# Performance work log

Hardware: AMD Instinct MI355X
Metric: run time of the kernel (lower is better)

The kernel has to match this reference:

```python
import jax, jax.numpy as jnp
import numpy as np

B, SEQ, D_TOK = 2, 2048, 1536
H, DH = 24, 64
TP, NS, NMH, DFLOW = 4, 256, 8, 64


def setup_inputs() -> dict:
    key = jax.random.key(0)
    ks = jax.random.split(key, 10)
    s = 0.02  # weight scale to keep activations sane
    return {
        "hidden_states": jax.random.normal(ks[0], (B, SEQ, D_TOK), jnp.float32),
        "Wq": jax.random.normal(ks[1], (D_TOK, D_TOK), jnp.float32) * s,
        "Wk": jax.random.normal(ks[2], (D_TOK, D_TOK), jnp.float32) * s,
        "Wv": jax.random.normal(ks[3], (D_TOK, D_TOK), jnp.float32) * s,
        "Wo": jax.random.normal(ks[4], (D_TOK, D_TOK), jnp.float32) * s,
        "bo": jnp.zeros((D_TOK,), jnp.float32),
        "M": jax.random.normal(ks[5], (B, TP, NS, DFLOW), jnp.float32),
        "W_region": jax.random.uniform(ks[6], (B, TP, NS, 1), jnp.float32),
        "Fk": jax.random.normal(ks[7], (NMH, DFLOW, DH), jnp.float32) * s,
        "Fv": jax.random.normal(ks[8], (NMH, DFLOW, DH), jnp.float32) * s,
    }


def reference(hidden_states, Wq, Wk, Wv, Wo, bo, M, W_region, Fk, Fv):
    # QKV projections, split into heads: [B, H, seq, Dh]
    Q = (hidden_states @ Wq).reshape(B, SEQ, H, DH).transpose(0, 2, 1, 3)
    K = (hidden_states @ Wk).reshape(B, SEQ, H, DH).transpose(0, 2, 1, 3)
    V = (hidden_states @ Wv).reshape(B, SEQ, H, DH).transpose(0, 2, 1, 3)

    # Motion injection (vectorized over b, h, t): region-gated flow deltas
    # delta[b,h,t,n,d] = W_region[b,t,n] * (M[b,t,n,:] @ Fk[h])
    gate = W_region[:, None]  # [B,1,TP,NS,1]
    dK = jnp.einsum('btnf,hfd->bhtnd', M, Fk) * gate  # [B,NMH,TP,NS,DH]
    dV = jnp.einsum('btnf,hfd->bhtnd', M, Fv) * gate

    # seq = 2 blocks (content, canny) x TP frames x NS spatial tokens;
    # delta is applied to both halves of each frame, first NMH heads only.
    K = K.reshape(B, H, 2, TP, NS, DH).at[:, :NMH].add(dK[:, :, None]).reshape(B, H, SEQ, DH)
    V = V.reshape(B, H, 2, TP, NS, DH).at[:, :NMH].add(dV[:, :, None]).reshape(B, H, SEQ, DH)

    # Standard SDPA
    scale = 1.0 / np.sqrt(DH).astype(np.float32)
    scores = jnp.einsum('bhqd,bhkd->bhqk', Q, K) * scale
    attn_w = jax.nn.softmax(scores, axis=-1)
    out = jnp.einsum('bhqk,bhkd->bhqd', attn_w, V)

    out = out.transpose(0, 2, 1, 3).reshape(B, SEQ, D_TOK)
    return out @ Wo + bo
```

## Files before the change

### kernel.cpp

```cpp
#include <hip/hip_runtime.h>
#include <hip/hip_bf16.h>

typedef __attribute__((ext_vector_type(4))) float f32x4;
typedef __attribute__((ext_vector_type(8))) short bf16x8;

#define LOG2E 1.4426950408889634f

__device__ __forceinline__ unsigned short f2b(float f) {
  union { float f; unsigned u; } v; v.f = f;
  unsigned r = v.u + 0x7fffu + ((v.u >> 16) & 1u);
  return (unsigned short)(r >> 16);
}
__device__ __forceinline__ float b2f(unsigned short s) {
  union { unsigned u; float f; } v; v.u = ((unsigned)s) << 16;
  return v.f;
}
__device__ __forceinline__ unsigned cvtpk(float lo, float hi) {
  unsigned r;
  asm("v_cvt_pk_bf16_f32 %0, %1, %2" : "=v"(r) : "v"(lo), "v"(hi));
  return r;
}
__device__ __forceinline__ float fexp2(float x) {
  float r;
  asm("v_exp_f32 %0, %1" : "=v"(r) : "v"(x));
  return r;
}

__device__ __forceinline__ void gload_lds16(const void* g, void* l) {
  __builtin_amdgcn_global_load_lds(
      (const __attribute__((address_space(1))) unsigned*)g,
      (__attribute__((address_space(3))) unsigned*)l, 16, 0, 0);
}

__global__ __launch_bounds__(256) void k_cvt(const float* __restrict__ src,
                                             unsigned short* __restrict__ dst, int n4) {
  int i = blockIdx.x * 256 + threadIdx.x;
  if (i >= n4) return;
  float4 v = ((const float4*)src)[i];
  ushort4 o;
  o.x = f2b(v.x); o.y = f2b(v.y); o.z = f2b(v.z); o.w = f2b(v.w);
  ((ushort4*)dst)[i] = o;
}

__global__ __launch_bounds__(256) void k_transpose(const float* __restrict__ src,
                                                   unsigned short* __restrict__ dst) {
  __shared__ float tile[64][65];
  const int tx = threadIdx.x & 63, ty = threadIdx.x >> 6;
  const int r0 = (blockIdx.x / 24) * 64, c0 = (blockIdx.x % 24) * 64;
#pragma unroll
  for (int j = 0; j < 16; ++j)
    tile[ty + j * 4][tx] = src[(size_t)(r0 + ty + j * 4) * 1536 + c0 + tx];
  __syncthreads();
#pragma unroll
  for (int j = 0; j < 16; ++j)
    dst[(size_t)(c0 + ty + j * 4) * 1536 + r0 + tx] = f2b(tile[tx][ty + j * 4]);
}

template <int OUTBF16>
__global__ __launch_bounds__(256) void k_gemm(const unsigned short* __restrict__ A,
                                              const unsigned short* __restrict__ BT,
                                              void* __restrict__ C,
                                              const float* __restrict__ bias,
                                              int M, int N, int K, int gridN) {
  __shared__ unsigned short As[128 * 32];
  __shared__ unsigned short Bs[128 * 32];
  const int tid = threadIdx.x;
  const int lane = tid & 63, wave = tid >> 6;
  const int bm = (blockIdx.x / gridN) * 128;
  const int bn = (blockIdx.x % gridN) * 128;
  const int wr = (wave >> 1) * 64, wc = (wave & 1) * 64;
  const int r15 = lane & 15, g = lane >> 4;
  const int row0 = tid >> 2, c0 = tid & 3;

  f32x4 acc[4][4] = {};

  for (int k0 = 0; k0 < K; k0 += 32) {
    __syncthreads();
    gload_lds16(A + (size_t)(bm + row0) * K + k0 + c0 * 8, (char*)As + wave * 1024);
    gload_lds16(A + (size_t)(bm + row0 + 64) * K + k0 + c0 * 8,
                (char*)As + 4096 + wave * 1024);
    gload_lds16(BT + (size_t)(bn + row0) * K + k0 + c0 * 8, (char*)Bs + wave * 1024);
    gload_lds16(BT + (size_t)(bn + row0 + 64) * K + k0 + c0 * 8,
                (char*)Bs + 4096 + wave * 1024);
    __syncthreads();
    bf16x8 af[4], bfr[4];
#pragma unroll
    for (int m = 0; m < 4; ++m) {
      af[m] = *(const bf16x8*)&As[(wr + m * 16 + r15) * 32 + g * 8];
      bfr[m] = *(const bf16x8*)&Bs[(wc + m * 16 + r15) * 32 + g * 8];
    }
#pragma unroll
    for (int m = 0; m < 4; ++m)
#pragma unroll
      for (int n = 0; n < 4; ++n)
        acc[m][n] = __builtin_amdgcn_mfma_f32_16x16x32_bf16(af[m], bfr[n], acc[m][n], 0, 0, 0);
  }

#pragma unroll
  for (int m = 0; m < 4; ++m)
#pragma unroll
    for (int n = 0; n < 4; ++n)
#pragma unroll
      for (int i = 0; i < 4; ++i) {
        int row = bm + wr + m * 16 + g * 4 + i;
        int col = bn + wc + n * 16 + r15;
        float v = acc[m][n][i];
        if (OUTBF16)
          ((unsigned short*)C)[(size_t)row * N + col] = f2b(v);
        else
          ((float*)C)[(size_t)row * N + col] = v + bias[col];
      }
}

__global__ __launch_bounds__(256) void k_inject(const float* __restrict__ Mm,
                                                const float* __restrict__ Wr,
                                                const float* __restrict__ Fk,
                                                const float* __restrict__ Fv,
                                                unsigned short* __restrict__ qkv) {
  __shared__ float Ml[256];
  __shared__ float gl[4];
  const int bid = blockIdx.x;
  const int nb = bid & 63, t = (bid >> 6) & 3, h = (bid >> 8) & 7, b = bid >> 11;
  const int tid = threadIdx.x;
  const int nl = tid >> 6, d = tid & 63;
  Ml[tid] = Mm[(size_t)(((b * 4 + t) * 256 + nb * 4) * 64) + tid];
  if (tid < 4) gl[tid] = Wr[(b * 4 + t) * 256 + nb * 4 + tid];
  __syncthreads();
  float ak = 0.f, av = 0.f;
#pragma unroll 8
  for (int f = 0; f < 64; ++f) {
    float mv = Ml[nl * 64 + f];
    ak += mv * Fk[(h * 64 + f) * 64 + d];
    av += mv * Fv[(h * 64 + f) * 64 + d];
  }
  float gate = gl[nl];
  ak *= gate; av *= gate;
  const int n = nb * 4 + nl;
  const size_t s0 = (size_t)(b * 2048 + t * 256 + n);
#pragma unroll
  for (int r = 0; r < 2; ++r) {
    size_t row = s0 + (size_t)r * 1024;
    size_t ik = row * 4608 + 1536 + h * 64 + d;
    qkv[ik] = f2b(b2f(qkv[ik]) + ak);
    size_t iv = row * 4608 + 3072 + h * 64 + d;
    qkv[iv] = f2b(b2f(qkv[iv]) + av);
  }
}

__global__ __launch_bounds__(512) void k_attn(const unsigned short* __restrict__ qkv,
                                              unsigned short* __restrict__ attno) {
  __shared__ unsigned short Kl[64 * 64];
  __shared__ unsigned short VT[64 * 72];
  __shared__ unsigned short Pl[8][16 * 72];
  const int tid = threadIdx.x;
  const int lane = tid & 63, wave = tid >> 6;
  const int bid = blockIdx.x;
  const int qt = bid & 15;
  const int h = (bid >> 4) % 24;
  const int b = (bid >> 4) / 24;
  const int r15 = lane & 15, g = lane >> 4, sw7 = lane & 7;
  const int q0 = qt * 128 + wave * 16;
  const size_t RS = 4608;
  const size_t tokbase = (size_t)(b * 2048);

  bf16x8 qb[2];
  {
    const unsigned short* qrow = qkv + (tokbase + q0 + r15) * RS + h * 64;
    const float qs = 0.125f * LOG2E;
#pragma unroll
    for (int kk = 0; kk < 2; ++kk) {
      bf16x8 v = *(const bf16x8*)(qrow + kk * 32 + g * 8);
#pragma unroll
      for (int e = 0; e < 8; ++e)
        v[e] = (short)f2b(b2f((unsigned short)v[e]) * qs);
      qb[kk] = v;
    }
  }

  f32x4 o[4] = {};
  float m_run = -1e30f, l_run = 0.0f;

  const int krow = tid >> 3, kc = tid & 7;
  const int ksc = kc ^ (krow & 7);

  for (int kv0 = 0; kv0 < 2048; kv0 += 64) {
    __syncthreads();
    gload_lds16(qkv + (tokbase + kv0 + krow) * RS + 1536 + h * 64 + ksc * 8,
                (char*)Kl + wave * 1024);
    bf16x8 vv = *(const bf16x8*)(qkv + (tokbase + kv0 + lane) * RS + 3072 + h * 64 + wave * 8);
#pragma unroll
    for (int e = 0; e < 8; ++e)
      VT[(wave * 8 + e) * 72 + lane] = (unsigned short)vv[e];
    __syncthreads();

    f32x4 st[4];
    __builtin_amdgcn_s_setprio(1);
#pragma unroll
    for (int m = 0; m < 4; ++m) {
      int row = m * 16 + r15;
      bf16x8 ka0 = *(const bf16x8*)&Kl[row * 64 + ((g ^ sw7) * 8)];
      bf16x8 ka1 = *(const bf16x8*)&Kl[row * 64 + (((g + 4) ^ sw7) * 8)];
      f32x4 z = {0.f, 0.f, 0.f, 0.f};
      st[m] = __builtin_amdgcn_mfma_f32_16x16x32_bf16(ka0, qb[0], z, 0, 0, 0);
      st[m] = __builtin_amdgcn_mfma_f32_16x16x32_bf16(ka1, qb[1], st[m], 0, 0, 0);
    }
    __builtin_amdgcn_s_setprio(0);

    float pm = fmaxf(fmaxf(fmaxf(st[0][0], st[0][1]), fmaxf(st[0][2], st[0][3])),
                     fmaxf(fmaxf(st[1][0], st[1][1]), fmaxf(st[1][2], st[1][3])));
    pm = fmaxf(pm,
               fmaxf(fmaxf(fmaxf(st[2][0], st[2][1]), fmaxf(st[2][2], st[2][3])),
                     fmaxf(fmaxf(st[3][0], st[3][1]), fmaxf(st[3][2], st[3][3]))));
    pm = fmaxf(pm, __shfl_xor(pm, 16, 64));
    pm = fmaxf(pm, __shfl_xor(pm, 32, 64));

    if (!__all(pm - m_run <= 8.0f)) {
      float mnew = fmaxf(m_run, pm);
      float fac = fexp2(m_run - mnew);
      l_run *= fac;
      float f_i[4];
#pragma unroll
      for (int i = 0; i < 4; ++i)
        f_i[i] = __shfl(fac, (lane & 48) | ((((lane >> 4) & 3) << 2) + i), 64);
#pragma unroll
      for (int dt = 0; dt < 4; ++dt)
#pragma unroll
        for (int i = 0; i < 4; ++i) o[dt][i] *= f_i[i];
      m_run = mnew;
    }

    float psum = 0.f;
#pragma unroll
    for (int m = 0; m < 4; ++m) {
      float p0 = fexp2(st[m][0] - m_run);
      float p1 = fexp2(st[m][1] - m_run);
      float p2 = fexp2(st[m][2] - m_run);
      float p3 = fexp2(st[m][3] - m_run);
      psum += (p0 + p1) + (p2 + p3);
      uint2 w2;
      w2.x = cvtpk(p0, p1);
      w2.y = cvtpk(p2, p3);
      *(uint2*)&Pl[wave][r15 * 72 + m * 16 + g * 4] = w2;
    }
    psum += __shfl_xor(psum, 16, 64);
    psum += __shfl_xor(psum, 32, 64);
    l_run += psum;

    __builtin_amdgcn_s_setprio(1);
#pragma unroll
    for (int kap = 0; kap < 2; ++kap) {
      bf16x8 pa = *(const bf16x8*)&Pl[wave][r15 * 72 + kap * 32 + g * 8];
#pragma unroll
      for (int dt = 0; dt < 4; ++dt) {
        bf16x8 vb = *(const bf16x8*)&VT[(dt * 16 + r15) * 72 + kap * 32 + g * 8];
        o[dt] = __builtin_amdgcn_mfma_f32_16x16x32_bf16(pa, vb, o[dt], 0, 0, 0);
      }
    }
    __builtin_amdgcn_s_setprio(0);
  }

  float rl = 1.0f / l_run;
  float r_i[4];
#pragma unroll
  for (int i = 0; i < 4; ++i)
    r_i[i] = __shfl(rl, (lane & 48) | ((((lane >> 4) & 3) << 2) + i), 64);
#pragma unroll
  for (int dt = 0; dt < 4; ++dt)
#pragma unroll
    for (int i = 0; i < 4; ++i) {
      int q = q0 + ((lane >> 4) << 2) + i;
      int col = h * 64 + dt * 16 + r15;
      attno[(tokbase + q) * 1536 + col] = f2b(o[dt][i] * r_i[i]);
    }
}

extern "C" void kernel_launch(void* const* d_in, const int* in_sizes, int n_in,
                              void* d_out, int out_size, void* d_ws, size_t ws_size,
                              hipStream_t stream) {
  const float* hs = (const float*)d_in[0];
  const float* Wq = (const float*)d_in[1];
  const float* Wk = (const float*)d_in[2];
  const float* Wv = (const float*)d_in[3];
  const float* Wo = (const float*)d_in[4];
  const float* bo = (const float*)d_in[5];
  const float* Mm = (const float*)d_in[6];
  const float* Wr = (const float*)d_in[7];
  const float* Fk = (const float*)d_in[8];
  const float* Fv = (const float*)d_in[9];
  float* out = (float*)d_out;

  unsigned short* hsb   = (unsigned short*)d_ws;
  unsigned short* wqkvt = hsb + (size_t)4096 * 1536;
  unsigned short* qkv   = wqkvt + (size_t)4608 * 1536;
  unsigned short* attno = hsb;
  unsigned short* wot   = wqkvt;

  k_cvt<<<6144, 256, 0, stream>>>(hs, hsb, 1572864);
  k_transpose<<<576, 256, 0, stream>>>(Wq, wqkvt);
  k_transpose<<<576, 256, 0, stream>>>(Wk, wqkvt + (size_t)1536 * 1536);
  k_transpose<<<576, 256, 0, stream>>>(Wv, wqkvt + (size_t)3072 * 1536);

  k_gemm<1><<<32 * 36, 256, 0, stream>>>(hsb, wqkvt, (void*)qkv, (const float*)nullptr,
                                         4096, 4608, 1536, 36);
  k_transpose<<<576, 256, 0, stream>>>(Wo, wot);
  k_inject<<<4096, 256, 0, stream>>>(Mm, Wr, Fk, Fv, qkv);
  k_attn<<<768, 512, 0, stream>>>(qkv, attno);
  k_gemm<0><<<32 * 12, 256, 0, stream>>>(attno, wot, (void*)out, bo, 4096, 1536, 1536, 12);
}
```

Before: 264.4 us.

## Double-buffer K/V tiles in attention, 32 queries per wave, merge QKV transposes

The attention kernel now runs 4 waves of 32 query rows each instead of 8 waves of 16. Each K fragment read from LDS is reused across two query sub-tiles. The K and V tiles are double-buffered so the next tile's global loads overlap the current tile's compute, which removes one barrier per iteration. The three weight transposes are also merged into one launch. In exchange, register pressure goes up and LDS use roughly doubles, which could lower occupancy.

```diff
diff --git a/kernel.cpp b/kernel.cpp
--- a/kernel.cpp
+++ b/kernel.cpp
@@ -40,6 +40,26 @@
   ushort4 o;
   o.x = f2b(v.x); o.y = f2b(v.y); o.z = f2b(v.z); o.w = f2b(v.w);
   ((ushort4*)dst)[i] = o;
+}
+
+__global__ __launch_bounds__(256) void k_transpose3(const float* __restrict__ s0,
+                                                    const float* __restrict__ s1,
+                                                    const float* __restrict__ s2,
+                                                    unsigned short* __restrict__ dst) {
+  __shared__ float tile[64][65];
+  const int which = blockIdx.x / 576;
+  const int bid = blockIdx.x % 576;
+  const float* src = which == 0 ? s0 : (which == 1 ? s1 : s2);
+  unsigned short* d = dst + (size_t)which * 1536 * 1536;
+  const int tx = threadIdx.x & 63, ty = threadIdx.x >> 6;
+  const int r0 = (bid / 24) * 64, c0 = (bid % 24) * 64;
+#pragma unroll
+  for (int j = 0; j < 16; ++j)
+    tile[ty + j * 4][tx] = src[(size_t)(r0 + ty + j * 4) * 1536 + c0 + tx];
+  __syncthreads();
+#pragma unroll
+  for (int j = 0; j < 16; ++j)
+    d[(size_t)(c0 + ty + j * 4) * 1536 + r0 + tx] = f2b(tile[tx][ty + j * 4]);
 }
 
 __global__ __launch_bounds__(256) void k_transpose(const float* __restrict__ src,
@@ -147,131 +167,193 @@
   }
 }
 
-__global__ __launch_bounds__(512) void k_attn(const unsigned short* __restrict__ qkv,
-                                              unsigned short* __restrict__ attno) {
-  __shared__ unsigned short Kl[64 * 64];
-  __shared__ unsigned short VT[64 * 72];
-  __shared__ unsigned short Pl[8][16 * 72];
+__global__ __launch_bounds__(256, 3) void k_attn(const unsigned short* __restrict__ qkv,
+                                                 unsigned short* __restrict__ attno) {
+  __shared__ unsigned short Kl[2 * 64 * 64];
+  __shared__ unsigned short VT[2 * 64 * 72];
+  __shared__ unsigned short Pl[4 * 32 * 72];
   const int tid = threadIdx.x;
   const int lane = tid & 63, wave = tid >> 6;
   const int bid = blockIdx.x;
   const int qt = bid & 15;
   const int h = (bid >> 4) % 24;
   const int b = (bid >> 4) / 24;
-  const int r15 = lane & 15, g = lane >> 4, sw7 = lane & 7;
-  const int q0 = qt * 128 + wave * 16;
+  const int r15 = lane & 15, g = lane >> 4;
+  const int q0 = qt * 128 + wave * 32;
   const size_t RS = 4608;
   const size_t tokbase = (size_t)(b * 2048);
-
-  bf16x8 qb[2];
+  unsigned short* Plw = Pl + wave * 32 * 72;
+
+  bf16x8 qb[2][2];
   {
-    const unsigned short* qrow = qkv + (tokbase + q0 + r15) * RS + h * 64;
     const float qs = 0.125f * LOG2E;
 #pragma unroll
-    for (int kk = 0; kk < 2; ++kk) {
-      bf16x8 v = *(const bf16x8*)(qrow + kk * 32 + g * 8);
-#pragma unroll
-      for (int e = 0; e < 8; ++e)
-        v[e] = (short)f2b(b2f((unsigned short)v[e]) * qs);
-      qb[kk] = v;
-    }
-  }
-
-  f32x4 o[4] = {};
-  float m_run = -1e30f, l_run = 0.0f;
-
-  const int krow = tid >> 3, kc = tid & 7;
-  const int ksc = kc ^ (krow & 7);
-
-  for (int kv0 = 0; kv0 < 2048; kv0 += 64) {
-    __syncthreads();
-    gload_lds16(qkv + (tokbase + kv0 + krow) * RS + 1536 + h * 64 + ksc * 8,
-                (char*)Kl + wave * 1024);
-    bf16x8 vv = *(const bf16x8*)(qkv + (tokbase + kv0 + lane) * RS + 3072 + h * 64 + wave * 8);
-#pragma unroll
-    for (int e = 0; e < 8; ++e)
-      VT[(wave * 8 + e) * 72 + lane] = (unsigned short)vv[e];
-    __syncthreads();
-
-    f32x4 st[4];
+    for (int qh = 0; qh < 2; ++qh) {
+      const unsigned short* qrow = qkv + (tokbase + q0 + qh * 16 + r15) * RS + h * 64;
+#pragma unroll
+      for (int kk = 0; kk < 2; ++kk) {
+        bf16x8 v = *(const bf16x8*)(qrow + kk * 32 + g * 8);
+#pragma unroll
+        for (int e = 0; e < 8; ++e)
+          v[e] = (short)f2b(b2f((unsigned short)v[e]) * qs);
+        qb[qh][kk] = v;
+      }
+    }
+  }
+
+  f32x4 o[2][4] = {};
+  float m_run[2] = {-1e30f, -1e30f}, l_run[2] = {0.f, 0.f};
+  bf16x8 vr[2];
+
+  const int ch0 = wave * 2 * 64 + lane, ch1 = (wave * 2 + 1) * 64 + lane;
+  const int kr0 = ch0 >> 3, kc0s = ((ch0 & 7) ^ (kr0 & 7)) * 8;
+  const int kr1 = ch1 >> 3, kc1s = ((ch1 & 7) ^ (kr1 & 7)) * 8;
+
+#define STAGE_K(buf, kv0)                                                          \
+  {                                                                                \
+    gload_lds16(qkv + (tokbase + (kv0) + kr0) * RS + 1536 + h * 64 + kc0s,         \
+                (char*)Kl + (buf) * 8192 + (wave * 2) * 1024);                     \
+    gload_lds16(qkv + (tokbase + (kv0) + kr1) * RS + 1536 + h * 64 + kc1s,         \
+                (char*)Kl + (buf) * 8192 + (wave * 2 + 1) * 1024);                 \
+  }
+#define LOAD_V(kv0)                                                                \
+  {                                                                                \
+    const unsigned short* vrow = qkv + (tokbase + (kv0) + lane) * RS + 3072 + h * 64; \
+    vr[0] = *(const bf16x8*)(vrow + (wave * 2) * 8);                               \
+    vr[1] = *(const bf16x8*)(vrow + (wave * 2 + 1) * 8);                           \
+  }
+#define WRITE_V(buf)                                                               \
+  {                                                                                \
+    _Pragma("unroll") for (int s = 0; s < 2; ++s) {                                \
+      int d0 = (wave * 2 + s) * 8;                                                 \
+      _Pragma("unroll") for (int e = 0; e < 8; ++e)                                \
+          VT[(buf) * 4608 + (d0 + e) * 72 + lane] = (unsigned short)vr[s][e];      \
+    }                                                                              \
+  }
+
+  STAGE_K(0, 0);
+  LOAD_V(0);
+  asm volatile("s_waitcnt vmcnt(0)" ::: "memory");
+  WRITE_V(0);
+  __syncthreads();
+
+  int cur = 0;
+  for (int t = 0; t < 32; ++t) {
+    const int kv0 = t * 64;
+    if (t < 31) {
+      STAGE_K(cur ^ 1, kv0 + 64);
+      LOAD_V(kv0 + 64);
+    }
+
+    f32x4 st[4][2];
+    const unsigned short* Kb = Kl + cur * 4096;
     __builtin_amdgcn_s_setprio(1);
 #pragma unroll
     for (int m = 0; m < 4; ++m) {
       int row = m * 16 + r15;
-      bf16x8 ka0 = *(const bf16x8*)&Kl[row * 64 + ((g ^ sw7) * 8)];
-      bf16x8 ka1 = *(const bf16x8*)&Kl[row * 64 + (((g + 4) ^ sw7) * 8)];
-      f32x4 z = {0.f, 0.f, 0.f, 0.f};
-      st[m] = __builtin_amdgcn_mfma_f32_16x16x32_bf16(ka0, qb[0], z, 0, 0, 0);
-      st[m] = __builtin_amdgcn_mfma_f32_16x16x32_bf16(ka1, qb[1], st[m], 0, 0, 0);
+      int r7 = row & 7;
+      bf16x8 ka0 = *(const bf16x8*)&Kb[row * 64 + ((g ^ r7) * 8)];
+      bf16x8 ka1 = *(const bf16x8*)&Kb[row * 64 + (((4 + g) ^ r7) * 8)];
+#pragma unroll
+      for (int qh = 0; qh < 2; ++qh) {
+        f32x4 z = {0.f, 0.f, 0.f, 0.f};
+        st[m][qh] = __builtin_amdgcn_mfma_f32_16x16x32_bf16(ka0, qb[qh][0], z, 0, 0, 0);
+        st[m][qh] = __builtin_amdgcn_mfma_f32_16x16x32_bf16(ka1, qb[qh][1], st[m][qh], 0, 0, 0);
+      }
     }
     __builtin_amdgcn_s_setprio(0);
 
-    float pm = fmaxf(fmaxf(fmaxf(st[0][0], st[0][1]), fmaxf(st[0][2], st[0][3])),
-                     fmaxf(fmaxf(st[1][0], st[1][1]), fmaxf(st[1][2], st[1][3])));
-    pm = fmaxf(pm,
-               fmaxf(fmaxf(fmaxf(st[2][0], st[2][1]), fmaxf(st[2][2], st[2][3])),
-                     fmaxf(fmaxf(st[3][0], st[3][1]), fmaxf(st[3][2], st[3][3]))));
-    pm = fmaxf(pm, __shfl_xor(pm, 16, 64));
-    pm = fmaxf(pm, __shfl_xor(pm, 32, 64));
-
-    if (!__all(pm - m_run <= 8.0f)) {
-      float mnew = fmaxf(m_run, pm);
-      float fac = fexp2(m_run - mnew);
-      l_run *= fac;
-      float f_i[4];
-#pragma unroll
-      for (int i = 0; i < 4; ++i)
-        f_i[i] = __shfl(fac, (lane & 48) | ((((lane >> 4) & 3) << 2) + i), 64);
-#pragma unroll
-      for (int dt = 0; dt < 4; ++dt)
-#pragma unroll
-        for (int i = 0; i < 4; ++i) o[dt][i] *= f_i[i];
-      m_run = mnew;
-    }
-
-    float psum = 0.f;
-#pragma unroll
-    for (int m = 0; m < 4; ++m) {
-      float p0 = fexp2(st[m][0] - m_run);
-      float p1 = fexp2(st[m][1] - m_run);
-      float p2 = fexp2(st[m][2] - m_run);
-      float p3 = fexp2(st[m][3] - m_run);
-      psum += (p0 + p1) + (p2 + p3);
-      uint2 w2;
-      w2.x = cvtpk(p0, p1);
-      w2.y = cvtpk(p2, p3);
-      *(uint2*)&Pl[wave][r15 * 72 + m * 16 + g * 4] = w2;
-    }
-    psum += __shfl_xor(psum, 16, 64);
-    psum += __shfl_xor(psum, 32, 64);
-    l_run += psum;
-
+    float pm[2];
+#pragma unroll
+    for (int qh = 0; qh < 2; ++qh) {
+      float p = fmaxf(fmaxf(fmaxf(st[0][qh][0], st[0][qh][1]), fmaxf(st[0][qh][2], st[0][qh][3])),
+                      fmaxf(fmaxf(st[1][qh][0], st[1][qh][1]), fmaxf(st[1][qh][2], st[1][qh][3])));
+      p = fmaxf(p,
+                fmaxf(fmaxf(fmaxf(st[2][qh][0], st[2][qh][1]), fmaxf(st[2][qh][2], st[2][qh][3])),
+                      fmaxf(fmaxf(st[3][qh][0], st[3][qh][1]), fmaxf(st[3][qh][2], st[3][qh][3]))));
+      p = fmaxf(p, __shfl_xor(p, 16, 64));
+      pm[qh] = fmaxf(p, __shfl_xor(p, 32, 64));
+    }
+
+    if (!__all(pm[0] - m_run[0] <= 8.0f && pm[1] - m_run[1] <= 8.0f)) {
+#pragma unroll
+      for (int qh = 0; qh < 2; ++qh) {
+        float mnew = fmaxf(m_run[qh], pm[qh]);
+        float fac = fexp2(m_run[qh] - mnew);
+        l_run[qh] *= fac;
+        float f_i[4];
+#pragma unroll
+        for (int i = 0; i < 4; ++i)
+          f_i[i] = __shfl(fac, (lane & 48) | ((((lane >> 4) & 3) << 2) + i), 64);
+#pragma unroll
+        for (int dt = 0; dt < 4; ++dt)
+#pragma unroll
+          for (int i = 0; i < 4; ++i) o[qh][dt][i] *= f_i[i];
+        m_run[qh] = mnew;
+      }
+    }
+
+    float psum[2] = {0.f, 0.f};
+#pragma unroll
+    for (int m = 0; m < 4; ++m)
+#pragma unroll
+      for (int qh = 0; qh < 2; ++qh) {
+        float p0 = fexp2(st[m][qh][0] - m_run[qh]);
+        float p1 = fexp2(st[m][qh][1] - m_run[qh]);
+        float p2 = fexp2(st[m][qh][2] - m_run[qh]);
+        float p3 = fexp2(st[m][qh][3] - m_run[qh]);
+        psum[qh] += (p0 + p1) + (p2 + p3);
+        uint2 w2;
+        w2.x = cvtpk(p0, p1);
+        w2.y = cvtpk(p2, p3);
+        *(uint2*)&Plw[(qh * 16 + r15) * 72 + m * 16 + g * 4] = w2;
+      }
+#pragma unroll
+    for (int qh = 0; qh < 2; ++qh) {
+      psum[qh] += __shfl_xor(psum[qh], 16, 64);
+      psum[qh] += __shfl_xor(psum[qh], 32, 64);
+      l_run[qh] += psum[qh];
+    }
+
+    const unsigned short* Vb = VT + cur * 4608;
     __builtin_amdgcn_s_setprio(1);
 #pragma unroll
     for (int kap = 0; kap < 2; ++kap) {
-      bf16x8 pa = *(const bf16x8*)&Pl[wave][r15 * 72 + kap * 32 + g * 8];
+      bf16x8 pa0 = *(const bf16x8*)&Plw[(r15) * 72 + kap * 32 + g * 8];
+      bf16x8 pa1 = *(const bf16x8*)&Plw[(16 + r15) * 72 + kap * 32 + g * 8];
 #pragma unroll
       for (int dt = 0; dt < 4; ++dt) {
-        bf16x8 vb = *(const bf16x8*)&VT[(dt * 16 + r15) * 72 + kap * 32 + g * 8];
-        o[dt] = __builtin_amdgcn_mfma_f32_16x16x32_bf16(pa, vb, o[dt], 0, 0, 0);
+        bf16x8 vb = *(const bf16x8*)&Vb[(dt * 16 + r15) * 72 + kap * 32 + g * 8];
+        o[0][dt] = __builtin_amdgcn_mfma_f32_16x16x32_bf16(pa0, vb, o[0][dt], 0, 0, 0);
+        o[1][dt] = __builtin_amdgcn_mfma_f32_16x16x32_bf16(pa1, vb, o[1][dt], 0, 0, 0);
       }
     }
     __builtin_amdgcn_s_setprio(0);
-  }
-
-  float rl = 1.0f / l_run;
-  float r_i[4];
-#pragma unroll
-  for (int i = 0; i < 4; ++i)
-    r_i[i] = __shfl(rl, (lane & 48) | ((((lane >> 4) & 3) << 2) + i), 64);
-#pragma unroll
-  for (int dt = 0; dt < 4; ++dt)
-#pragma unroll
-    for (int i = 0; i < 4; ++i) {
-      int q = q0 + ((lane >> 4) << 2) + i;
-      int col = h * 64 + dt * 16 + r15;
-      attno[(tokbase + q) * 1536 + col] = f2b(o[dt][i] * r_i[i]);
-    }
+
+    if (t < 31) {
+      asm volatile("s_waitcnt vmcnt(0)" ::: "memory");
+      WRITE_V(cur ^ 1);
+    }
+    __syncthreads();
+    cur ^= 1;
+  }
+
+#pragma unroll
+  for (int qh = 0; qh < 2; ++qh) {
+    float rl = 1.0f / l_run[qh];
+    float r_i[4];
+#pragma unroll
+    for (int i = 0; i < 4; ++i)
+      r_i[i] = __shfl(rl, (lane & 48) | ((((lane >> 4) & 3) << 2) + i), 64);
+#pragma unroll
+    for (int dt = 0; dt < 4; ++dt)
+#pragma unroll
+      for (int i = 0; i < 4; ++i) {
+        int q = q0 + qh * 16 + ((lane >> 4) << 2) + i;
+        int col = h * 64 + dt * 16 + r15;
+        attno[(tokbase + q) * 1536 + col] = f2b(o[qh][dt][i] * r_i[i]);
+      }
+  }
 }
 
 extern "C" void kernel_launch(void* const* d_in, const int* in_sizes, int n_in,
@@ -296,14 +378,12 @@
   unsigned short* wot   = wqkvt;
 
   k_cvt<<<6144, 256, 0, stream>>>(hs, hsb, 1572864);
-  k_transpose<<<576, 256, 0, stream>>>(Wq, wqkvt);
-  k_transpose<<<576, 256, 0, stream>>>(Wk, wqkvt + (size_t)1536 * 1536);
-  k_transpose<<<576, 256, 0, stream>>>(Wv, wqkvt + (size_t)3072 * 1536);
+  k_transpose3<<<1728, 256, 0, stream>>>(Wq, Wk, Wv, wqkvt);
 
   k_gemm<1><<<32 * 36, 256, 0, stream>>>(hsb, wqkvt, (void*)qkv, (const float*)nullptr,
                                          4096, 4608, 1536, 36);
   k_transpose<<<576, 256, 0, stream>>>(Wo, wot);
   k_inject<<<4096, 256, 0, stream>>>(Mm, Wr, Fk, Fv, qkv);
-  k_attn<<<768, 512, 0, stream>>>(qkv, attno);
+  k_attn<<<768, 256, 0, stream>>>(qkv, attno);
   k_gemm<0><<<32 * 12, 256, 0, stream>>>(attno, wot, (void*)out, bo, 4096, 1536, 1536, 12);
 }
```

Result: faster. 252.3 us (-4.6%).
